# Performance work log

Hardware: AMD Instinct MI355X
Metric: run time of the kernel (lower is better)

## Reference

```python
import jax, jax.numpy as jnp
import numpy as np

B, T_IN, FEAT, UNITS, OUT_STEPS = 2048, 48, 64, 1024, 64


def setup_inputs() -> dict:
    key = jax.random.key(0)
    k0, k1, k2, k3 = jax.random.split(key, 4)
    inputs = jax.random.normal(k0, (B, T_IN, FEAT), dtype=jnp.float32)
    # glorot-ish scaling so gates don't saturate immediately
    W = jax.random.normal(k1, (FEAT, 4 * UNITS), dtype=jnp.float32) / np.sqrt(FEAT)
    U = jax.random.normal(k2, (UNITS, 4 * UNITS), dtype=jnp.float32) / np.sqrt(UNITS)
    b = jnp.zeros((4 * UNITS,), dtype=jnp.float32)
    Wd = jax.random.normal(k3, (UNITS, FEAT), dtype=jnp.float32) / np.sqrt(UNITS)
    bd = jnp.zeros((FEAT,), dtype=jnp.float32)
    return {"inputs": inputs, "W": W, "U": U, "b": b, "Wd": Wd, "bd": bd}


def _lstm_cell(h, c, x, W, U, b):
    # Keras LSTMCell gate order: i, f, g(candidate), o
    z = x @ W + h @ U + b  # [B, 4*units]
    i, f, g, o = jnp.split(z, 4, axis=-1)
    c = jax.nn.sigmoid(f) * c + jax.nn.sigmoid(i) * jnp.tanh(g)
    h = jax.nn.sigmoid(o) * jnp.tanh(c)
    return h, c


def reference(inputs, W, U, b, Wd, bd):
    batch = inputs.shape[0]
    units = U.shape[0]
    h0 = jnp.zeros((batch, units), dtype=inputs.dtype)
    c0 = jnp.zeros((batch, units), dtype=inputs.dtype)

    # warmup: run LSTM over the input sequence (time-major scan)
    def warm_step(carry, x_t):
        h, c = carry
        h, c = _lstm_cell(h, c, x_t, W, U, b)
        return (h, c), None

    (h, c), _ = jax.lax.scan(warm_step, (h0, c0), jnp.swapaxes(inputs, 0, 1))
    pred = h @ Wd + bd  # first prediction, [B, feat]

    def dec_step(carry, _):
        h, c, p = carry
        h, c = _lstm_cell(h, c, p, W, U, b)
        p = h @ Wd + bd
        return (h, c, p), p

    _, preds = jax.lax.scan(dec_step, (h, c, pred), None, length=OUT_STEPS - 1)
    preds = jnp.concatenate([pred[None], preds], axis=0)  # [out_steps, B, feat]
    return jnp.swapaxes(preds, 0, 1)  # [B, out_steps, feat]
```

## Files before the change

### kernel.cpp

```cpp
#include <hip/hip_runtime.h>
#include <hip/hip_bf16.h>

typedef float f32x4 __attribute__((ext_vector_type(4)));
typedef __bf16 bf16x8 __attribute__((ext_vector_type(8)));

#define B_SZ 2048
#define T_IN 48
#define FEAT 64
#define UNITS 1024
#define GCOLS 4096
#define OUT_STEPS 64
#define KWARM 1088

__device__ __forceinline__ int oc_of(int c) {
    return (((c >> 4) & 3) * UNITS) + ((c >> 6) * 16) + (c & 15);
}

typedef __attribute__((address_space(1))) const void gas_t;
typedef __attribute__((address_space(3))) void las_t;

__device__ __forceinline__ void gl_lds16(const void* g, void* l) {
    __builtin_amdgcn_global_load_lds((gas_t*)g, (las_t*)l, 16, 0, 0);
}
__device__ __forceinline__ float sigm(float x) {
    return __builtin_amdgcn_rcpf(1.0f + __expf(-x));
}
__device__ __forceinline__ float tanh_fast(float x) {
    float e = __expf(2.0f * x);
    return 1.0f - 2.0f * __builtin_amdgcn_rcpf(e + 1.0f);
}


__global__ __launch_bounds__(256) void reorder_UW(const float* __restrict__ U, const float* __restrict__ W,
                                                  __hip_bfloat16* __restrict__ UTw) {
    __shared__ __hip_bfloat16 t[64][64];
    const int k0 = blockIdx.x * 64;
    const int c0 = blockIdx.y * 64;
    const int tid = threadIdx.x;
#pragma unroll
    for (int i = 0; i < 16; ++i) {
        int idx = tid + i * 256;
        int rk = idx >> 6, cc = idx & 63;
        int k = k0 + rk, c = c0 + cc;
        int oc = oc_of(c);
        float v = (k < UNITS) ? U[(size_t)k * GCOLS + oc] : W[(size_t)(k - UNITS) * GCOLS + oc];
        t[rk][cc] = __float2bfloat16(v);
    }
    __syncthreads();
#pragma unroll
    for (int i = 0; i < 16; ++i) {
        int idx = tid + i * 256;
        int rc = idx >> 6, kk = idx & 63;
        UTw[(size_t)(c0 + rc) * KWARM + k0 + kk] = t[kk][rc];
    }
}

__global__ __launch_bounds__(256) void transpose_Wd(const float* __restrict__ Wd, __hip_bfloat16* __restrict__ WdT) {
    __shared__ __hip_bfloat16 t[64][64];
    const int k0 = blockIdx.x * 64;
    const int tid = threadIdx.x;
#pragma unroll
    for (int i = 0; i < 16; ++i) {
        int idx = tid + i * 256;
        int rk = idx >> 6, ff = idx & 63;
        t[rk][ff] = __float2bfloat16(Wd[(size_t)(k0 + rk) * FEAT + ff]);
    }
    __syncthreads();
#pragma unroll
    for (int i = 0; i < 16; ++i) {
        int idx = tid + i * 256;
        int rf = idx >> 6, kk = idx & 63;
        WdT[(size_t)rf * UNITS + k0 + kk] = t[kk][rf];
    }
}

__global__ __launch_bounds__(256) void build_UTdec(const __hip_bfloat16* __restrict__ UTw,
                                                   const __hip_bfloat16* __restrict__ WdT,
                                                   __hip_bfloat16* __restrict__ UTd) {
    __shared__ float Wl[64][16];
    const int k = blockIdx.x * 256 + threadIdx.x;
    const int c0 = blockIdx.y * 16;
    const int tid = threadIdx.x;
#pragma unroll
    for (int i = 0; i < 4; ++i) {
        int idx = tid + i * 256;
        int f = idx >> 4, cc = idx & 15;
        Wl[f][cc] = __bfloat162float(UTw[(size_t)(c0 + cc) * KWARM + UNITS + f]);
    }
    __syncthreads();
    float acc[16];
#pragma unroll
    for (int cc = 0; cc < 16; ++cc) acc[cc] = 0.f;
    for (int f = 0; f < 64; ++f) {
        float wd = __bfloat162float(WdT[(size_t)f * UNITS + k]);
#pragma unroll
        for (int cc = 0; cc < 16; ++cc) acc[cc] += wd * Wl[f][cc];
    }
#pragma unroll
    for (int cc = 0; cc < 16; ++cc) {
        float uv = __bfloat162float(UTw[(size_t)(c0 + cc) * KWARM + k]);
        UTd[(size_t)(c0 + cc) * UNITS + k] = __float2bfloat16(uv + acc[cc]);
    }
}

__global__ __launch_bounds__(256) void build_bias(const float* __restrict__ b, const float* __restrict__ bd,
                                                  const __hip_bfloat16* __restrict__ UTw,
                                                  float* __restrict__ bw, float* __restrict__ bdc) {
    const int c = blockIdx.x * 256 + threadIdx.x;
    const int oc = oc_of(c);
    float base = b[oc];
    float s = 0.f;
    for (int f = 0; f < FEAT; ++f) s += bd[f] * __bfloat162float(UTw[(size_t)c * KWARM + UNITS + f]);
    bw[c] = base;
    bdc[c] = base + s;
}

__global__ void convert_x(const float* __restrict__ x, __hip_bfloat16* __restrict__ xb, int n) {
    int i = blockIdx.x * blockDim.x + threadIdx.x;
    if (i < n) xb[i] = __float2bfloat16(x[i]);
}

template <bool WARM, bool PRED>
__global__ __launch_bounds__(256) void lstm_step(
    const __hip_bfloat16* __restrict__ hin,
    const __hip_bfloat16* __restrict__ xbf, int t,
    const __hip_bfloat16* __restrict__ UT,
    const float* __restrict__ bias,
    __hip_bfloat16* __restrict__ cst,
    __hip_bfloat16* __restrict__ hout,
    const __hip_bfloat16* __restrict__ WdT,
    const float* __restrict__ bd,
    float* __restrict__ out, int tstep)
{
    constexpr int KD = WARM ? KWARM : UNITS;
    constexpr int NKT = KD / 64;

    __shared__ alignas(16) __hip_bfloat16 Al[2 * 8192];
    __shared__ alignas(16) __hip_bfloat16 Bl[2 * 8192];

    const int tid = threadIdx.x;
    const int lane = tid & 63;
    const int wv = tid >> 6;
    const int wr = wv >> 1, wc = wv & 1;
    const int bid = blockIdx.x;
    const int x = bid & 7;
    const int i6 = bid >> 3;
    const int mb = ((x >> 2) << 3) + (i6 >> 3);
    const int nb = ((x & 3) << 3) + (i6 & 7);
    const int m0 = mb * 128;
    const int n0 = nb * 128;
    const bool doPred = PRED && (nb < 4);

    f32x4 acc[4][4] = {};
    f32x4 accp[2] = {};

    const int lrow = lane >> 3;
    const int scol = ((lane & 7) * 16) ^ (lrow << 4);

    const char* aS[4]; const char* bS[4]; const char* xS[4];
#pragma unroll
    for (int r = 0; r < 4; ++r) {
        int row = (r * 4 + wv) * 8 + lrow;
        aS[r] = (const char*)hin + (size_t)(m0 + row) * (UNITS * 2) + scol;
        bS[r] = (const char*)UT + (size_t)(n0 + row) * (KD * 2) + scol;
        if (WARM) xS[r] = (const char*)xbf + (size_t)(m0 + row) * (T_IN * FEAT * 2) + (size_t)t * (FEAT * 2) + scol;
    }

    const int ar = lane & 15;
    const int ko = (lane >> 4) << 3;
    const int swz = (ar & 7) << 3;

    const char* wB = nullptr;
    if (PRED && doPred)
        wB = (const char*)WdT + ((size_t)(16 * nb + ar) * UNITS + ko) * 2;

    const int u16 = lane & 15;
    const int unit = (nb * 2 + wc) * 16 + u16;
    const int rbase = m0 + 64 * wr + ((lane >> 4) << 2);
    float bv[4];
#pragma unroll
    for (int g = 0; g < 4; ++g) bv[g] = bias[n0 + 64 * wc + 16 * g + u16];
    float bdv = 0.f;
    if (PRED && doPred) bdv = bd[16 * nb + u16];

    auto stage = [&](int kt) {
        const int buf = kt & 1;
#pragma unroll
        for (int r = 0; r < 4; ++r) {
            const char* s = (WARM && kt == NKT - 1) ? xS[r] : (aS[r] + kt * 128);
            gl_lds16(s, (char*)Al + buf * 16384 + (r * 4 + wv) * 1024);
        }
#pragma unroll
        for (int r = 0; r < 4; ++r)
            gl_lds16(bS[r] + kt * 128, (char*)Bl + buf * 16384 + (r * 4 + wv) * 1024);
    };

    bf16x8 Wf[2][2];
    auto loadWf = [&](int kt) {
        if (PRED && doPred) {
#pragma unroll
            for (int kk = 0; kk < 2; ++kk)
                Wf[kt & 1][kk] = *reinterpret_cast<const bf16x8*>(wB + kt * 128 + kk * 64);
        }
    };

    auto compute = [&](int kt) {
        const int buf = kt & 1;
#pragma unroll
        for (int kk = 0; kk < 2; ++kk) {
            bf16x8 af[4], bfr[4];
#pragma unroll
            for (int mi = 0; mi < 4; ++mi)
                af[mi] = *reinterpret_cast<const bf16x8*>(&Al[buf * 8192 + (64 * wr + 16 * mi + ar) * 64 + ((32 * kk + ko) ^ swz)]);
#pragma unroll
            for (int ni = 0; ni < 4; ++ni)
                bfr[ni] = *reinterpret_cast<const bf16x8*>(&Bl[buf * 8192 + (64 * wc + 16 * ni + ar) * 64 + ((32 * kk + ko) ^ swz)]);
#pragma unroll
            for (int mi = 0; mi < 4; ++mi)
#pragma unroll
                for (int ni = 0; ni < 4; ++ni)
                    acc[mi][ni] = __builtin_amdgcn_mfma_f32_16x16x32_bf16(af[mi], bfr[ni], acc[mi][ni], 0, 0, 0);
            if (PRED && doPred) {
#pragma unroll
                for (int pi = 0; pi < 2; ++pi)
                    accp[pi] = __builtin_amdgcn_mfma_f32_16x16x32_bf16(af[2 * wc + pi], Wf[kt & 1][kk], accp[pi], 0, 0, 0);
            }
        }
    };

    stage(0);
    loadWf(0);
#pragma unroll
    for (int kt = 0; kt < NKT - 1; ++kt) {
        stage(kt + 1);
        loadWf(kt + 1);
        if (PRED && doPred) asm volatile("s_waitcnt vmcnt(10) lgkmcnt(0)" ::: "memory");
        else                asm volatile("s_waitcnt vmcnt(8) lgkmcnt(0)" ::: "memory");
        __builtin_amdgcn_s_barrier();
        compute(kt);
        __builtin_amdgcn_s_barrier();
    }
    float cv[16];
#pragma unroll
    for (int mi = 0; mi < 4; ++mi)
#pragma unroll
        for (int reg = 0; reg < 4; ++reg)
            cv[mi * 4 + reg] = __bfloat162float(cst[(size_t)(rbase + 16 * mi + reg) * UNITS + unit]);
    asm volatile("s_waitcnt vmcnt(16) lgkmcnt(0)" ::: "memory");
    __builtin_amdgcn_s_barrier();
    compute(NKT - 1);

#pragma unroll
    for (int mi = 0; mi < 4; ++mi)
#pragma unroll
        for (int reg = 0; reg < 4; ++reg) {
            float zi = acc[mi][0][reg] + bv[0];
            float zf = acc[mi][1][reg] + bv[1];
            float zg = acc[mi][2][reg] + bv[2];
            float zo = acc[mi][3][reg] + bv[3];
            float cn = sigm(zf) * cv[mi * 4 + reg] + sigm(zi) * tanh_fast(zg);
            size_t idx = (size_t)(rbase + 16 * mi + reg) * UNITS + unit;
            cst[idx] = __float2bfloat16(cn);
            hout[idx] = __float2bfloat16(sigm(zo) * tanh_fast(cn));
        }

    if (PRED && doPred) {
#pragma unroll
        for (int pi = 0; pi < 2; ++pi) {
            const int prow = m0 + 64 * wr + 32 * wc + 16 * pi + ((lane >> 4) << 2);
            f32x4 v = accp[pi];
#pragma unroll
            for (int reg = 0; reg < 4; ++reg)
                out[(size_t)(prow + reg) * (OUT_STEPS * FEAT) + (size_t)tstep * FEAT + (16 * nb + u16)] = v[reg] + bdv;
        }
    }
}

extern "C" void kernel_launch(void* const* d_in, const int* in_sizes, int n_in,
                              void* d_out, int out_size, void* d_ws, size_t ws_size,
                              hipStream_t stream) {
    const float* inputs = (const float*)d_in[0];
    const float* W  = (const float*)d_in[1];
    const float* U  = (const float*)d_in[2];
    const float* b  = (const float*)d_in[3];
    const float* Wd = (const float*)d_in[4];
    const float* bd = (const float*)d_in[5];
    float* out = (float*)d_out;

    char* ws = (char*)d_ws;
    size_t off = 0;
    auto alloc = [&](size_t bytes) { char* p = ws + off; off = (off + bytes + 255) & ~255ULL; return p; };
    __hip_bfloat16* UTw = (__hip_bfloat16*)alloc((size_t)GCOLS * KWARM * 2);
    __hip_bfloat16* UTd = (__hip_bfloat16*)alloc((size_t)GCOLS * UNITS * 2);
    __hip_bfloat16* WdT = (__hip_bfloat16*)alloc((size_t)FEAT * UNITS * 2);
    __hip_bfloat16* Xbf = (__hip_bfloat16*)alloc((size_t)B_SZ * T_IN * FEAT * 2);
    __hip_bfloat16* hA  = (__hip_bfloat16*)alloc((size_t)B_SZ * UNITS * 2);
    __hip_bfloat16* hB  = (__hip_bfloat16*)alloc((size_t)B_SZ * UNITS * 2);
    __hip_bfloat16* cst = (__hip_bfloat16*)alloc((size_t)B_SZ * UNITS * 2);
    float* bw  = (float*)alloc(GCOLS * 4);
    float* bdc = (float*)alloc(GCOLS * 4);

    hipMemsetAsync(cst, 0, (size_t)B_SZ * UNITS * 2, stream);
    hipMemsetAsync(hA, 0, (size_t)B_SZ * UNITS * 2, stream);

    dim3 blk(256);
    reorder_UW<<<dim3(17, 64), blk, 0, stream>>>(U, W, UTw);
    transpose_Wd<<<dim3(16), blk, 0, stream>>>(Wd, WdT);
    build_UTdec<<<dim3(4, 256), blk, 0, stream>>>(UTw, WdT, UTd);
    build_bias<<<dim3(16), blk, 0, stream>>>(b, bd, UTw, bw, bdc);
    {
        int n = B_SZ * T_IN * FEAT;
        convert_x<<<dim3((n + 255) / 256), blk, 0, stream>>>(inputs, Xbf, n);
    }

    const __hip_bfloat16* cur = hA;
    __hip_bfloat16* nxt = hB;
    for (int t = 0; t < T_IN; ++t) {
        lstm_step<true, false><<<dim3(512), blk, 0, stream>>>(cur, Xbf, t, UTw, bw, cst, nxt,
                                                              nullptr, nullptr, nullptr, 0);
        __hip_bfloat16* tmp = (__hip_bfloat16*)cur; cur = nxt; nxt = tmp;
    }
    for (int t = 1; t <= OUT_STEPS; ++t) {
        lstm_step<false, true><<<dim3(512), blk, 0, stream>>>(cur, nullptr, 0, UTd, bdc, cst, nxt,
                                                              WdT, bd, out, t - 1);
        __hip_bfloat16* tmp = (__hip_bfloat16*)cur; cur = nxt; nxt = tmp;
    }
}
```

Measured before the change: 4.998 ms.

## Fuse four LSTM timesteps per launch using per-row-group global barriers

Result: slower. 14.73 ms (+194.8%).

```diff
diff --git a/kernel.cpp b/kernel.cpp
--- a/kernel.cpp
+++ b/kernel.cpp
@@ -28,6 +28,24 @@
 __device__ __forceinline__ float tanh_fast(float x) {
     float e = __expf(2.0f * x);
     return 1.0f - 2.0f * __builtin_amdgcn_rcpf(e + 1.0f);
+}
+
+__device__ __forceinline__ int group_barrier(int* cnt, int target) {
+    __threadfence();
+    __syncthreads();
+    __shared__ int ok_s;
+    if (threadIdx.x == 0) {
+        atomicAdd(cnt, 1);
+        int ok = 1, spins = 0;
+        while (__hip_atomic_load(cnt, __ATOMIC_RELAXED, __HIP_MEMORY_SCOPE_AGENT) < target) {
+            __builtin_amdgcn_s_sleep(4);
+            if (++spins > (1 << 20)) { ok = 0; atomicAdd(cnt, 1 << 20); break; }
+        }
+        ok_s = ok;
+    }
+    __syncthreads();
+    __threadfence();
+    return ok_s;
 }
 
 
@@ -121,16 +139,17 @@
 }
 
 template <bool WARM, bool PRED>
-__global__ __launch_bounds__(256) void lstm_step(
-    const __hip_bfloat16* __restrict__ hin,
-    const __hip_bfloat16* __restrict__ xbf, int t,
+__global__ __launch_bounds__(256) void lstm_step4(
+    __hip_bfloat16* __restrict__ hA,
+    __hip_bfloat16* __restrict__ hB,
+    const __hip_bfloat16* __restrict__ xbf, int t0,
     const __hip_bfloat16* __restrict__ UT,
     const float* __restrict__ bias,
     __hip_bfloat16* __restrict__ cst,
-    __hip_bfloat16* __restrict__ hout,
     const __hip_bfloat16* __restrict__ WdT,
     const float* __restrict__ bd,
-    float* __restrict__ out, int tstep)
+    float* __restrict__ out, int tstep0,
+    int* __restrict__ sync_cnt, int sbase)
 {
     constexpr int KD = WARM ? KWARM : UNITS;
     constexpr int NKT = KD / 64;
@@ -150,20 +169,18 @@
     const int m0 = mb * 128;
     const int n0 = nb * 128;
     const bool doPred = PRED && (nb < 4);
-
-    f32x4 acc[4][4] = {};
-    f32x4 accp[2] = {};
+    int* grp = sync_cnt + mb * 32;
 
     const int lrow = lane >> 3;
     const int scol = ((lane & 7) * 16) ^ (lrow << 4);
 
-    const char* aS[4]; const char* bS[4]; const char* xS[4];
+    size_t aOff[4]; const char* bS[4]; const char* xB[4];
 #pragma unroll
     for (int r = 0; r < 4; ++r) {
         int row = (r * 4 + wv) * 8 + lrow;
-        aS[r] = (const char*)hin + (size_t)(m0 + row) * (UNITS * 2) + scol;
+        aOff[r] = (size_t)(m0 + row) * (UNITS * 2) + scol;
         bS[r] = (const char*)UT + (size_t)(n0 + row) * (KD * 2) + scol;
-        if (WARM) xS[r] = (const char*)xbf + (size_t)(m0 + row) * (T_IN * FEAT * 2) + (size_t)t * (FEAT * 2) + scol;
+        if (WARM) xB[r] = (const char*)xbf + (size_t)(m0 + row) * (T_IN * FEAT * 2) + scol;
     }
 
     const int ar = lane & 15;
@@ -183,96 +200,113 @@
     float bdv = 0.f;
     if (PRED && doPred) bdv = bd[16 * nb + u16];
 
-    auto stage = [&](int kt) {
-        const int buf = kt & 1;
-#pragma unroll
-        for (int r = 0; r < 4; ++r) {
-            const char* s = (WARM && kt == NKT - 1) ? xS[r] : (aS[r] + kt * 128);
-            gl_lds16(s, (char*)Al + buf * 16384 + (r * 4 + wv) * 1024);
+    int healthy = 1;
+
+#pragma unroll 1
+    for (int j = 0; j < 4; ++j) {
+        const char* hin = (const char*)((j & 1) ? hB : hA);
+        __hip_bfloat16* hout = (j & 1) ? hA : hB;
+        const char* aS[4];
+#pragma unroll
+        for (int r = 0; r < 4; ++r) aS[r] = hin + aOff[r];
+        const int xoff = WARM ? (t0 + j) * (FEAT * 2) : 0;
+
+        f32x4 acc[4][4] = {};
+        f32x4 accp[2] = {};
+        bf16x8 Wf[2][2];
+
+        auto stage = [&](int kt) {
+            const int buf = kt & 1;
+#pragma unroll
+            for (int r = 0; r < 4; ++r) {
+                const char* s = (WARM && kt == NKT - 1) ? (xB[r] + xoff) : (aS[r] + kt * 128);
+                gl_lds16(s, (char*)Al + buf * 16384 + (r * 4 + wv) * 1024);
+            }
+#pragma unroll
+            for (int r = 0; r < 4; ++r)
+                gl_lds16(bS[r] + kt * 128, (char*)Bl + buf * 16384 + (r * 4 + wv) * 1024);
+        };
+        auto loadWf = [&](int kt) {
+            if (PRED && doPred) {
+#pragma unroll
+                for (int kk = 0; kk < 2; ++kk)
+                    Wf[kt & 1][kk] = *reinterpret_cast<const bf16x8*>(wB + kt * 128 + kk * 64);
+            }
+        };
+        auto compute = [&](int kt) {
+            const int buf = kt & 1;
+#pragma unroll
+            for (int kk = 0; kk < 2; ++kk) {
+                bf16x8 af[4], bfr[4];
+#pragma unroll
+                for (int mi = 0; mi < 4; ++mi)
+                    af[mi] = *reinterpret_cast<const bf16x8*>(&Al[buf * 8192 + (64 * wr + 16 * mi + ar) * 64 + ((32 * kk + ko) ^ swz)]);
+#pragma unroll
+                for (int ni = 0; ni < 4; ++ni)
+                    bfr[ni] = *reinterpret_cast<const bf16x8*>(&Bl[buf * 8192 + (64 * wc + 16 * ni + ar) * 64 + ((32 * kk + ko) ^ swz)]);
+#pragma unroll
+                for (int mi = 0; mi < 4; ++mi)
+#pragma unroll
+                    for (int ni = 0; ni < 4; ++ni)
+                        acc[mi][ni] = __builtin_amdgcn_mfma_f32_16x16x32_bf16(af[mi], bfr[ni], acc[mi][ni], 0, 0, 0);
+                if (PRED && doPred) {
+#pragma unroll
+                    for (int pi = 0; pi < 2; ++pi)
+                        accp[pi] = __builtin_amdgcn_mfma_f32_16x16x32_bf16(af[2 * wc + pi], Wf[kt & 1][kk], accp[pi], 0, 0, 0);
+                }
+            }
+        };
+
+        stage(0);
+        loadWf(0);
+#pragma unroll
+        for (int kt = 0; kt < NKT - 1; ++kt) {
+            stage(kt + 1);
+            loadWf(kt + 1);
+            if (PRED && doPred) asm volatile("s_waitcnt vmcnt(10) lgkmcnt(0)" ::: "memory");
+            else                asm volatile("s_waitcnt vmcnt(8) lgkmcnt(0)" ::: "memory");
+            __builtin_amdgcn_s_barrier();
+            compute(kt);
+            __builtin_amdgcn_s_barrier();
         }
-#pragma unroll
-        for (int r = 0; r < 4; ++r)
-            gl_lds16(bS[r] + kt * 128, (char*)Bl + buf * 16384 + (r * 4 + wv) * 1024);
-    };
-
-    bf16x8 Wf[2][2];
-    auto loadWf = [&](int kt) {
+        float cv[16];
+#pragma unroll
+        for (int mi = 0; mi < 4; ++mi)
+#pragma unroll
+            for (int reg = 0; reg < 4; ++reg)
+                cv[mi * 4 + reg] = __bfloat162float(cst[(size_t)(rbase + 16 * mi + reg) * UNITS + unit]);
+        asm volatile("s_waitcnt vmcnt(16) lgkmcnt(0)" ::: "memory");
+        __builtin_amdgcn_s_barrier();
+        compute(NKT - 1);
+
+#pragma unroll
+        for (int mi = 0; mi < 4; ++mi)
+#pragma unroll
+            for (int reg = 0; reg < 4; ++reg) {
+                float zi = acc[mi][0][reg] + bv[0];
+                float zf = acc[mi][1][reg] + bv[1];
+                float zg = acc[mi][2][reg] + bv[2];
+                float zo = acc[mi][3][reg] + bv[3];
+                float cn = sigm(zf) * cv[mi * 4 + reg] + sigm(zi) * tanh_fast(zg);
+                size_t idx = (size_t)(rbase + 16 * mi + reg) * UNITS + unit;
+                cst[idx] = __float2bfloat16(cn);
+                hout[idx] = __float2bfloat16(sigm(zo) * tanh_fast(cn));
+            }
+
         if (PRED && doPred) {
-#pragma unroll
-            for (int kk = 0; kk < 2; ++kk)
-                Wf[kt & 1][kk] = *reinterpret_cast<const bf16x8*>(wB + kt * 128 + kk * 64);
+            const int tstep = tstep0 + j;
+#pragma unroll
+            for (int pi = 0; pi < 2; ++pi) {
+                const int prow = m0 + 64 * wr + 32 * wc + 16 * pi + ((lane >> 4) << 2);
+                f32x4 v = accp[pi];
+#pragma unroll
+                for (int reg = 0; reg < 4; ++reg)
+                    out[(size_t)(prow + reg) * (OUT_STEPS * FEAT) + (size_t)tstep * FEAT + (16 * nb + u16)] = v[reg] + bdv;
+            }
         }
-    };
-
-    auto compute = [&](int kt) {
-        const int buf = kt & 1;
-#pragma unroll
-        for (int kk = 0; kk < 2; ++kk) {
-            bf16x8 af[4], bfr[4];
-#pragma unroll
-            for (int mi = 0; mi < 4; ++mi)
-                af[mi] = *reinterpret_cast<const bf16x8*>(&Al[buf * 8192 + (64 * wr + 16 * mi + ar) * 64 + ((32 * kk + ko) ^ swz)]);
-#pragma unroll
-            for (int ni = 0; ni < 4; ++ni)
-                bfr[ni] = *reinterpret_cast<const bf16x8*>(&Bl[buf * 8192 + (64 * wc + 16 * ni + ar) * 64 + ((32 * kk + ko) ^ swz)]);
-#pragma unroll
-            for (int mi = 0; mi < 4; ++mi)
-#pragma unroll
-                for (int ni = 0; ni < 4; ++ni)
-                    acc[mi][ni] = __builtin_amdgcn_mfma_f32_16x16x32_bf16(af[mi], bfr[ni], acc[mi][ni], 0, 0, 0);
-            if (PRED && doPred) {
-#pragma unroll
-                for (int pi = 0; pi < 2; ++pi)
-                    accp[pi] = __builtin_amdgcn_mfma_f32_16x16x32_bf16(af[2 * wc + pi], Wf[kt & 1][kk], accp[pi], 0, 0, 0);
-            }
-        }
-    };
-
-    stage(0);
-    loadWf(0);
-#pragma unroll
-    for (int kt = 0; kt < NKT - 1; ++kt) {
-        stage(kt + 1);
-        loadWf(kt + 1);
-        if (PRED && doPred) asm volatile("s_waitcnt vmcnt(10) lgkmcnt(0)" ::: "memory");
-        else                asm volatile("s_waitcnt vmcnt(8) lgkmcnt(0)" ::: "memory");
-        __builtin_amdgcn_s_barrier();
-        compute(kt);
-        __builtin_amdgcn_s_barrier();
-    }
-    float cv[16];
-#pragma unroll
-    for (int mi = 0; mi < 4; ++mi)
-#pragma unroll
-        for (int reg = 0; reg < 4; ++reg)
-            cv[mi * 4 + reg] = __bfloat162float(cst[(size_t)(rbase + 16 * mi + reg) * UNITS + unit]);
-    asm volatile("s_waitcnt vmcnt(16) lgkmcnt(0)" ::: "memory");
-    __builtin_amdgcn_s_barrier();
-    compute(NKT - 1);
-
-#pragma unroll
-    for (int mi = 0; mi < 4; ++mi)
-#pragma unroll
-        for (int reg = 0; reg < 4; ++reg) {
-            float zi = acc[mi][0][reg] + bv[0];
-            float zf = acc[mi][1][reg] + bv[1];
-            float zg = acc[mi][2][reg] + bv[2];
-            float zo = acc[mi][3][reg] + bv[3];
-            float cn = sigm(zf) * cv[mi * 4 + reg] + sigm(zi) * tanh_fast(zg);
-            size_t idx = (size_t)(rbase + 16 * mi + reg) * UNITS + unit;
-            cst[idx] = __float2bfloat16(cn);
-            hout[idx] = __float2bfloat16(sigm(zo) * tanh_fast(cn));
-        }
-
-    if (PRED && doPred) {
-#pragma unroll
-        for (int pi = 0; pi < 2; ++pi) {
-            const int prow = m0 + 64 * wr + 32 * wc + 16 * pi + ((lane >> 4) << 2);
-            f32x4 v = accp[pi];
-#pragma unroll
-            for (int reg = 0; reg < 4; ++reg)
-                out[(size_t)(prow + reg) * (OUT_STEPS * FEAT) + (size_t)tstep * FEAT + (16 * nb + u16)] = v[reg] + bdv;
-        }
+
+        if (j < 3 && healthy)
+            healthy = group_barrier(grp, 32 * (sbase + j + 1));
     }
 }
 
@@ -299,9 +333,11 @@
     __hip_bfloat16* cst = (__hip_bfloat16*)alloc((size_t)B_SZ * UNITS * 2);
     float* bw  = (float*)alloc(GCOLS * 4);
     float* bdc = (float*)alloc(GCOLS * 4);
+    int* sync_cnt = (int*)alloc(4096);
 
     hipMemsetAsync(cst, 0, (size_t)B_SZ * UNITS * 2, stream);
     hipMemsetAsync(hA, 0, (size_t)B_SZ * UNITS * 2, stream);
+    hipMemsetAsync(sync_cnt, 0, 4096, stream);
 
     dim3 blk(256);
     reorder_UW<<<dim3(17, 64), blk, 0, stream>>>(U, W, UTw);
@@ -313,16 +349,14 @@
         convert_x<<<dim3((n + 255) / 256), blk, 0, stream>>>(inputs, Xbf, n);
     }
 
-    const __hip_bfloat16* cur = hA;
-    __hip_bfloat16* nxt = hB;
-    for (int t = 0; t < T_IN; ++t) {
-        lstm_step<true, false><<<dim3(512), blk, 0, stream>>>(cur, Xbf, t, UTw, bw, cst, nxt,
-                                                              nullptr, nullptr, nullptr, 0);
-        __hip_bfloat16* tmp = (__hip_bfloat16*)cur; cur = nxt; nxt = tmp;
-    }
-    for (int t = 1; t <= OUT_STEPS; ++t) {
-        lstm_step<false, true><<<dim3(512), blk, 0, stream>>>(cur, nullptr, 0, UTd, bdc, cst, nxt,
-                                                              WdT, bd, out, t - 1);
-        __hip_bfloat16* tmp = (__hip_bfloat16*)cur; cur = nxt; nxt = tmp;
-    }
-}
+    for (int d = 0; d < 12; ++d) {
+        lstm_step4<true, false><<<dim3(512), blk, 0, stream>>>(
+            hA, hB, Xbf, 4 * d, UTw, bw, cst, nullptr, nullptr, nullptr, 0,
+            sync_cnt, 3 * d);
+    }
+    for (int d = 0; d < 16; ++d) {
+        lstm_step4<false, true><<<dim3(512), blk, 0, stream>>>(
+            hA, hB, nullptr, 0, UTd, bdc, cst, WdT, bd, out, 4 * d,
+            sync_cnt, 3 * (12 + d));
+    }
+}
```
